# Optimization experiments

Measured on AMD Instinct MI355X. Metric: run time of the kernel, lower is better.

The kernel has to match this reference:

```python
import jax, jax.numpy as jnp
import numpy as np

TOKEN_SIZE = 4
NEIGHBOR_SIZE = 3


def setup_inputs() -> dict:
    key = jax.random.key(0)
    ks = jax.random.split(key, 8)
    B, C, H, W = 8, 256, 64, 64
    return {
        "blue_feat": jax.random.normal(ks[0], (B, C, H, W), jnp.float32),
        "white_feat": jax.random.normal(ks[1], (B, C, H, W), jnp.float32),
        "Wq": jax.random.normal(ks[2], (C, C), jnp.float32) * 0.05,
        "bq": jax.random.normal(ks[3], (C,), jnp.float32) * 0.05,
        "Wk": jax.random.normal(ks[4], (C, C), jnp.float32) * 0.05,
        "bk": jax.random.normal(ks[5], (C,), jnp.float32) * 0.05,
        "Wv": jax.random.normal(ks[6], (C, C), jnp.float32) * 0.05,
        "bv": jax.random.normal(ks[7], (C,), jnp.float32) * 0.05,
    }


def _tokens(x, nh, nw, ts):
    # [B,C,H,W] -> [B,nh,nw,C,ts*ts]
    B, C = x.shape[0], x.shape[1]
    return (x.reshape(B, C, nh, ts, nw, ts)
             .transpose(0, 2, 4, 1, 3, 5)
             .reshape(B, nh, nw, C, ts * ts))


def reference(blue_feat, white_feat, Wq, bq, Wk, bk, Wv, bv):
    ts, ns = TOKEN_SIZE, NEIGHBOR_SIZE
    pad = ns // 2
    B, C, H, W = blue_feat.shape
    scale = float((ts * ts) ** -0.5)

    # 1x1 conv projections (pointwise channel mix + bias)
    Q = jnp.einsum('bchw,oc->bohw', blue_feat, Wq) + bq[None, :, None, None]
    K = jnp.einsum('bchw,oc->bohw', white_feat, Wk) + bk[None, :, None, None]
    V = jnp.einsum('bchw,oc->bohw', white_feat, Wv) + bv[None, :, None, None]

    nh, nw = H // ts, W // ts  # H,W divisible by ts -> no padding branch
    Qt = _tokens(Q, nh, nw, ts)  # [B,nh,nw,C,D]
    Kt = _tokens(K, nh, nw, ts)
    Vt = _tokens(V, nh, nw, ts)

    # zero-padded token grid, gather 3x3 neighbor tokens (F.unfold equivalent)
    padw = ((0, 0), (pad, pad), (pad, pad), (0, 0), (0, 0))
    Kp = jnp.pad(Kt, padw)
    Vp = jnp.pad(Vt, padw)
    Knb = jnp.stack([Kp[:, di:di + nh, dj:dj + nw]
                     for di in range(ns) for dj in range(ns)], axis=3)  # [B,nh,nw,9,C,D]
    Vnb = jnp.stack([Vp[:, di:di + nh, dj:dj + nw]
                     for di in range(ns) for dj in range(ns)], axis=3)

    # per-channel attention over neighbor tokens
    attn = jax.nn.softmax(
        jnp.einsum('bhwcd,bhwncd->bhwcn', Qt, Knb) * scale, axis=-1)
    out = jnp.einsum('bhwcn,bhwncd->bhwcd', attn, Vnb)  # [B,nh,nw,C,D]

    enhanced = (out.reshape(B, nh, nw, C, ts, ts)
                   .transpose(0, 3, 1, 4, 2, 5)
                   .reshape(B, C, H, W))
    return blue_feat + enhanced  # out_proj is Identity since c1 == c2
```

## Files before the change

kernel.cpp:

```cpp
#include <hip/hip_runtime.h>
#include <hip/hip_bf16.h>
#include <stdint.h>

typedef float  f32x4  __attribute__((ext_vector_type(4)));
typedef float  f32x2  __attribute__((ext_vector_type(2)));
typedef __bf16 bf16x8 __attribute__((ext_vector_type(8)));

#define LROW 40

__global__ __launch_bounds__(256) void wprep_kernel(
    const float* __restrict__ Wq, const float* __restrict__ Wk,
    const float* __restrict__ Wv, __bf16* __restrict__ Wbf)
{
  const int wb = blockIdx.x;
  const int t  = wb >> 5;
  const float* src = (t == 0) ? Wq : (t == 1) ? Wk : Wv;
  const int off = (wb & 31) * 2048 + threadIdx.x * 8;
  f32x4 v0 = *(const f32x4*)(src + off);
  f32x4 v1 = *(const f32x4*)(src + off + 4);
  bf16x8 r;
#pragma unroll
  for (int q = 0; q < 4; ++q) { r[q] = (__bf16)v0[q]; r[q + 4] = (__bf16)v1[q]; }
  *(bf16x8*)(Wbf + t * 65536 + off) = r;
}


#define GLOAD16(GS, LD) \
  __builtin_amdgcn_global_load_lds( \
      (const __attribute__((address_space(1))) uint32_t*)(GS), \
      (__attribute__((address_space(3))) uint32_t*)(LD), 16, 0, 0)

__global__ __launch_bounds__(256) void gemm_f32lds_kernel(
    const float* __restrict__ blue, const float* __restrict__ white,
    const __bf16* __restrict__ Wbf,
    const float* __restrict__ bq, const float* __restrict__ bk,
    const float* __restrict__ bv,
    __bf16* __restrict__ Qt, __bf16* __restrict__ Kt, __bf16* __restrict__ Vt)
{
  __shared__ float  Bsf[3][32 * 128];
  __shared__ __bf16 As[3][128 * 32];

  const int bid = blockIdx.x;
  const int lid = (bid & 7) * 192 + (bid >> 3);
  const int nb  = lid / 6;
  const int bt  = lid % 6;
  const int tensor = (bt < 4) ? 1 + (bt & 1) : 0;
  const int ob     = (bt < 4) ? (bt >> 1) : (bt & 1);

  const float*  X    = (tensor == 0) ? blue : white;
  const float*  bias = (tensor == 0) ? bq : (tensor == 1) ? bk : bv;
  __bf16*       Out  = (tensor == 0) ? Qt : (tensor == 1) ? Kt : Vt;
  const __bf16* Wp   = Wbf + tensor * 65536 + ob * 32768;

  const int tid  = threadIdx.x;
  const int lane = tid & 63;
  const int w    = tid >> 6;
  const int wo   = w >> 1;
  const int wn   = w & 1;
  const int lrow = lane & 15;
  const int lks  = lane >> 4;

  const int o0    = ob * 128;
  const int n0    = nb * 128;
  const int batch = n0 >> 12;
  const int p0    = n0 & 4095;
  const int tk0   = p0 >> 4;
  const int trow  = tk0 >> 4;
  const int tcol0 = tk0 & 15;
  const float* Xb = X + (size_t)batch * (256 * 4096);

  const float* gB[4];
#pragma unroll
  for (int m = 0; m < 4; ++m) {
    const int c      = m * 4 + w;
    const int krow   = 2 * c + (lane >> 5);
    const int g      = c >> 2;
    const int px_src = ((lane & 31) * 4 + 16 * g) & 127;
    const int tl     = px_src >> 4;
    const int d      = px_src & 15;
    const int hw     = (trow * 4 + (d >> 2)) * 64 + (tcol0 + tl) * 4 + (d & 3);
    gB[m] = Xb + (size_t)krow * 4096 + hw;
  }

  const int rA    = w * 16 + (lane >> 2);
  const int gslot = (lane & 3) ^ ((lane >> 3) & 3);
  const __bf16* gA = Wp + (size_t)rA * 256 + gslot * 8;
  const int ldsOffQ0 = (w * 16) * 32;
  const int ldsOffQ1 = (64 + w * 16) * 32;

#define STAGE(BUF, KK) do {                                          \
    GLOAD16(gA + (KK) * 32,            &As[BUF][ldsOffQ0]);          \
    GLOAD16(gA + 64 * 256 + (KK) * 32, &As[BUF][ldsOffQ1]);          \
    GLOAD16(gB[0] + (size_t)(KK) * 32 * 4096, &Bsf[BUF][(0 * 4 + w) * 256]); \
    GLOAD16(gB[1] + (size_t)(KK) * 32 * 4096, &Bsf[BUF][(1 * 4 + w) * 256]); \
    GLOAD16(gB[2] + (size_t)(KK) * 32 * 4096, &Bsf[BUF][(2 * 4 + w) * 256]); \
    GLOAD16(gB[3] + (size_t)(KK) * 32 * 4096, &Bsf[BUF][(3 * 4 + w) * 256]); \
  } while (0)

  const int sxA = (lks ^ ((lrow >> 1) & 3)) * 8;
  const int pxb = wn * 64 + lrow;

  f32x4 acc[4][4];
#pragma unroll
  for (int i = 0; i < 4; ++i)
#pragma unroll
    for (int j = 0; j < 4; ++j) acc[i][j] = (f32x4)0.0f;

#define COMPUTE(BUF) do {                                                       \
    bf16x8 af[4], bfr[4];                                                       \
    _Pragma("unroll")                                                           \
    for (int i = 0; i < 4; ++i)                                                 \
      af[i] = *(const bf16x8*)&As[BUF][(wo * 64 + i * 16 + lrow) * 32 + sxA];   \
    _Pragma("unroll")                                                           \
    for (int j = 0; j < 4; ++j) {                                               \
      const int s = (pxb + j * 16 - 16 * lks + 128) & 127;                      \
      const float* bp = &Bsf[BUF][lks * 8 * 128 + s];                           \
      bf16x8 v;                                                                 \
      _Pragma("unroll")                                                         \
      for (int kk = 0; kk < 8; ++kk) v[kk] = (__bf16)bp[kk * 128];              \
      bfr[j] = v;                                                               \
    }                                                                           \
    __builtin_amdgcn_s_setprio(1);                                              \
    _Pragma("unroll")                                                           \
    for (int i = 0; i < 4; ++i)                                                 \
      _Pragma("unroll")                                                         \
      for (int j = 0; j < 4; ++j)                                               \
        acc[i][j] = __builtin_amdgcn_mfma_f32_16x16x32_bf16(af[i], bfr[j],      \
                                                            acc[i][j], 0, 0, 0);\
    __builtin_amdgcn_s_setprio(0);                                              \
  } while (0)

  STAGE(0, 0);
  STAGE(1, 1);
  STAGE(2, 2);

#define PHASE(T) do {                                                           \
    if ((T) == 7)      asm volatile("s_waitcnt vmcnt(0)"  ::: "memory");        \
    else if ((T) == 6) asm volatile("s_waitcnt vmcnt(6)"  ::: "memory");        \
    else               asm volatile("s_waitcnt vmcnt(12)" ::: "memory");        \
    __builtin_amdgcn_sched_barrier(0);                                          \
    __builtin_amdgcn_s_barrier();                                               \
    __builtin_amdgcn_sched_barrier(0);                                          \
    COMPUTE((T) % 3);                                                           \
    asm volatile("s_waitcnt lgkmcnt(0)" ::: "memory");                          \
    __builtin_amdgcn_sched_barrier(0);                                          \
    __builtin_amdgcn_s_barrier();                                               \
    __builtin_amdgcn_sched_barrier(0);                                          \
    if ((T) < 5) STAGE((T) % 3, (T) + 3);                                       \
  } while (0)

  PHASE(0); PHASE(1); PHASE(2); PHASE(3);
  PHASE(4); PHASE(5); PHASE(6); PHASE(7);
#undef PHASE
#undef STAGE
#undef COMPUTE

#pragma unroll
  for (int i = 0; i < 4; ++i) {
    const int obase = o0 + wo * 64 + i * 16 + (lane >> 4) * 4;
#pragma unroll
    for (int j = 0; j < 4; ++j) {
      const int n  = n0 + wn * 64 + j * 16 + (lane & 15);
      const int bb = n >> 12;
      const int pp = n & 4095;
      const int tt = pp >> 4;
      const int tii = tt >> 4;
      const int tjj = tt & 15;
      const int dd  = pp & 15;
      const size_t base = ((size_t)(bb * 16 + tii) * 256) * 256 + tjj * 16 + dd;
#pragma unroll
      for (int r = 0; r < 4; ++r) {
        const int o = obase + r;
        const float v = acc[i][j][r] + bias[o];
        Out[base + (size_t)o * 256] = (__bf16)v;
      }
    }
  }
}

__global__ __launch_bounds__(256) void proj_gemm_kernel(
    const float* __restrict__ blue, const float* __restrict__ white,
    const float* __restrict__ Wq, const float* __restrict__ bq,
    const float* __restrict__ Wk, const float* __restrict__ bk,
    const float* __restrict__ Wv, const float* __restrict__ bv,
    __bf16* __restrict__ Qt, __bf16* __restrict__ Kt, __bf16* __restrict__ Vt)
{
  __shared__ __bf16 As[128 * LROW];
  __shared__ __bf16 Bs[128 * LROW];

  const int bidhw = blockIdx.x;
  const int lid   = (bidhw & 7) * 192 + (bidhw >> 3);
  const int nb    = lid / 6;
  const int bt    = lid % 6;
  const int tensor = (bt < 4) ? 1 + (bt & 1) : 0;
  const int ob     = (bt < 4) ? (bt >> 1) : (bt & 1);

  const float* X    = (tensor == 0) ? blue : white;
  const float* W    = (tensor == 0) ? Wq : (tensor == 1) ? Wk : Wv;
  const float* bias = (tensor == 0) ? bq : (tensor == 1) ? bk : bv;
  __bf16*      Out  = (tensor == 0) ? Qt : (tensor == 1) ? Kt : Vt;

  const int tid  = threadIdx.x;
  const int lane = tid & 63;
  const int wave = tid >> 6;
  const int wo   = wave >> 1;
  const int wn   = wave & 1;

  const int o0 = ob * 128;
  const int n0 = nb * 128;
  const int batch = n0 >> 12;
  const int p0    = n0 & 4095;
  const int tk0   = p0 >> 4;
  const int trow  = tk0 >> 4;
  const int tcol0 = tk0 & 15;
  const float* Xb = X + (size_t)batch * (256 * 4096);

  f32x4 acc[4][4];
#pragma unroll
  for (int i = 0; i < 4; ++i)
#pragma unroll
    for (int j = 0; j < 4; ++j) acc[i][j] = (f32x4)0.0f;

  const int arow  = tid >> 1;
  const int ahalf = tid & 1;
  const int n2   = tid & 63;
  const int ko   = tid >> 6;
  const int nloc = 2 * n2;
  const int tl   = nloc >> 4;
  const int d    = nloc & 15;
  const int hw   = (trow * 4 + (d >> 2)) * 64 + (tcol0 + tl) * 4 + (d & 3);

  const int lrow = lane & 15;
  const int lk   = (lane >> 4) * 8;

  for (int kk = 0; kk < 8; ++kk) {
    const int k0 = kk * 32;
    {
      const float* src = W + (size_t)(o0 + arow) * 256 + k0 + ahalf * 16;
      f32x4 t0 = *(const f32x4*)(src + 0);
      f32x4 t1 = *(const f32x4*)(src + 4);
      f32x4 t2 = *(const f32x4*)(src + 8);
      f32x4 t3 = *(const f32x4*)(src + 12);
      bf16x8 c0, c1;
#pragma unroll
      for (int qq = 0; qq < 4; ++qq) { c0[qq] = (__bf16)t0[qq]; c0[qq + 4] = (__bf16)t1[qq]; }
#pragma unroll
      for (int qq = 0; qq < 4; ++qq) { c1[qq] = (__bf16)t2[qq]; c1[qq + 4] = (__bf16)t3[qq]; }
      __bf16* dst = As + arow * LROW + ahalf * 16;
      *(bf16x8*)(dst + 0) = c0;
      *(bf16x8*)(dst + 8) = c1;
    }
    {
      const float* src = Xb + (size_t)(k0 + ko * 8) * 4096 + hw;
      f32x2 v0 = *(const f32x2*)(src + 0 * 4096);
      f32x2 v1 = *(const f32x2*)(src + 1 * 4096);
      f32x2 v2 = *(const f32x2*)(src + 2 * 4096);
      f32x2 v3 = *(const f32x2*)(src + 3 * 4096);
      f32x2 v4 = *(const f32x2*)(src + 4 * 4096);
      f32x2 v5 = *(const f32x2*)(src + 5 * 4096);
      f32x2 v6 = *(const f32x2*)(src + 6 * 4096);
      f32x2 v7 = *(const f32x2*)(src + 7 * 4096);
      bf16x8 r0, r1;
      r0[0] = (__bf16)v0[0]; r0[1] = (__bf16)v1[0]; r0[2] = (__bf16)v2[0]; r0[3] = (__bf16)v3[0];
      r0[4] = (__bf16)v4[0]; r0[5] = (__bf16)v5[0]; r0[6] = (__bf16)v6[0]; r0[7] = (__bf16)v7[0];
      r1[0] = (__bf16)v0[1]; r1[1] = (__bf16)v1[1]; r1[2] = (__bf16)v2[1]; r1[3] = (__bf16)v3[1];
      r1[4] = (__bf16)v4[1]; r1[5] = (__bf16)v5[1]; r1[6] = (__bf16)v6[1]; r1[7] = (__bf16)v7[1];
      *(bf16x8*)(Bs + (nloc + 0) * LROW + ko * 8) = r0;
      *(bf16x8*)(Bs + (nloc + 1) * LROW + ko * 8) = r1;
    }
    __syncthreads();

    bf16x8 a[4], b[4];
#pragma unroll
    for (int i = 0; i < 4; ++i)
      a[i] = *(const bf16x8*)(As + (wo * 64 + i * 16 + lrow) * LROW + lk);
#pragma unroll
    for (int j = 0; j < 4; ++j)
      b[j] = *(const bf16x8*)(Bs + (wn * 64 + j * 16 + lrow) * LROW + lk);
#pragma unroll
    for (int i = 0; i < 4; ++i)
#pragma unroll
      for (int j = 0; j < 4; ++j)
        acc[i][j] = __builtin_amdgcn_mfma_f32_16x16x32_bf16(a[i], b[j], acc[i][j], 0, 0, 0);
    __syncthreads();
  }

#pragma unroll
  for (int i = 0; i < 4; ++i) {
    const int obase = o0 + wo * 64 + i * 16 + (lane >> 4) * 4;
#pragma unroll
    for (int j = 0; j < 4; ++j) {
      const int n  = n0 + wn * 64 + j * 16 + (lane & 15);
      const int bb = n >> 12;
      const int p  = n & 4095;
      const int tt = p >> 4;
      const int tii = tt >> 4;
      const int tjj = tt & 15;
      const int dd  = p & 15;
      const size_t base = ((size_t)(bb * 16 + tii) * 256) * 256 + tjj * 16 + dd;
#pragma unroll
      for (int r = 0; r < 4; ++r) {
        const int o = obase + r;
        const float v = acc[i][j][r] + bias[o];
        Out[base + (size_t)o * 256] = (__bf16)v;
      }
    }
  }
}

__device__ __forceinline__ void unpack8(const uint4 v, float* f) {
  const uint32_t u0 = v.x, u1 = v.y, u2 = v.z, u3 = v.w;
  f[0] = __uint_as_float(u0 << 16); f[1] = __uint_as_float(u0 & 0xffff0000u);
  f[2] = __uint_as_float(u1 << 16); f[3] = __uint_as_float(u1 & 0xffff0000u);
  f[4] = __uint_as_float(u2 << 16); f[5] = __uint_as_float(u2 & 0xffff0000u);
  f[6] = __uint_as_float(u3 << 16); f[7] = __uint_as_float(u3 & 0xffff0000u);
}

__global__ __launch_bounds__(256) void attn_kernel(
    const __bf16* __restrict__ Qt, const __bf16* __restrict__ Kt,
    const __bf16* __restrict__ Vt, const float* __restrict__ blue,
    float* __restrict__ out)
{
  const int j   = blockIdx.x;
  const int bid = (j & 7) * 256 + (j >> 3);
  const int cg  = bid & 15;
  const int ti  = (bid >> 4) & 15;
  const int b   = bid >> 8;

  const int tid = threadIdx.x;
  const int tj  = tid & 15;
  const int cl  = tid >> 4;
  const int c   = cg * 16 + cl;

  float q[16];
  {
    const __bf16* p = Qt + ((((size_t)b * 16 + ti) * 256 + c) * 16 + tj) * 16;
    unpack8(*(const uint4*)p, q);
    unpack8(*(const uint4*)(p + 8), q + 8);
  }

  float s[9];
#pragma unroll
  for (int n = 0; n < 9; ++n) {
    const int yi = ti + n / 3 - 1;
    const int yj = tj + n % 3 - 1;
    float dot = 0.0f;
    if (yi >= 0 && yi < 16 && yj >= 0 && yj < 16) {
      const __bf16* p = Kt + ((((size_t)b * 16 + yi) * 256 + c) * 16 + yj) * 16;
      float kf[16];
      unpack8(*(const uint4*)p, kf);
      unpack8(*(const uint4*)(p + 8), kf + 8);
#pragma unroll
      for (int dd = 0; dd < 16; ++dd) dot = fmaf(q[dd], kf[dd], dot);
    }
    s[n] = dot * 0.25f;
  }

  float m = s[0];
#pragma unroll
  for (int n = 1; n < 9; ++n) m = fmaxf(m, s[n]);
  float w[9], denom = 0.0f;
#pragma unroll
  for (int n = 0; n < 9; ++n) { w[n] = __expf(s[n] - m); denom += w[n]; }
  const float inv = 1.0f / denom;

  float o16[16];
#pragma unroll
  for (int dd = 0; dd < 16; ++dd) o16[dd] = 0.0f;
#pragma unroll
  for (int n = 0; n < 9; ++n) {
    const int yi = ti + n / 3 - 1;
    const int yj = tj + n % 3 - 1;
    if (yi >= 0 && yi < 16 && yj >= 0 && yj < 16) {
      const __bf16* p = Vt + ((((size_t)b * 16 + yi) * 256 + c) * 16 + yj) * 16;
      float vf[16];
      unpack8(*(const uint4*)p, vf);
      unpack8(*(const uint4*)(p + 8), vf + 8);
#pragma unroll
      for (int dd = 0; dd < 16; ++dd) o16[dd] = fmaf(w[n], vf[dd], o16[dd]);
    }
  }

  const size_t pbase = ((size_t)b * 256 + c) * 4096 + (size_t)(ti * 4) * 64 + tj * 4;
#pragma unroll
  for (int r = 0; r < 4; ++r) {
    f32x4 bl = *(const f32x4*)(blue + pbase + r * 64);
    f32x4 ov;
#pragma unroll
    for (int j2 = 0; j2 < 4; ++j2) ov[j2] = bl[j2] + o16[r * 4 + j2] * inv;
    *(f32x4*)(out + pbase + r * 64) = ov;
  }
}

extern "C" void kernel_launch(void* const* d_in, const int* in_sizes, int n_in,
                              void* d_out, int out_size, void* d_ws, size_t ws_size,
                              hipStream_t stream) {
  const float* blue  = (const float*)d_in[0];
  const float* white = (const float*)d_in[1];
  const float* Wq = (const float*)d_in[2];
  const float* bq = (const float*)d_in[3];
  const float* Wk = (const float*)d_in[4];
  const float* bk = (const float*)d_in[5];
  const float* Wv = (const float*)d_in[6];
  const float* bv = (const float*)d_in[7];
  float* out = (float*)d_out;

  const size_t tsz = (size_t)8 * 256 * 256 * 16;
  __bf16* Qt = (__bf16*)d_ws;
  __bf16* Kt = Qt + tsz;
  __bf16* Vt = Kt + tsz;

  const size_t need = (3 * tsz + 3 * 65536) * sizeof(__bf16);
  if (ws_size >= need) {
    __bf16* Wbf = Vt + tsz;
    wprep_kernel<<<96, 256, 0, stream>>>(Wq, Wk, Wv, Wbf);
    gemm_f32lds_kernel<<<1536, 256, 0, stream>>>(blue, white, Wbf, bq, bk, bv, Qt, Kt, Vt);
  } else {
    proj_gemm_kernel<<<1536, 256, 0, stream>>>(blue, white, Wq, bq, Wk, bk, Wv, bv, Qt, Kt, Vt);
  }
  attn_kernel<<<2048, 256, 0, stream>>>(Qt, Kt, Vt, blue, out);
}
```

Before: 72.69 us.

## Transpose fp32 B tile to padded bf16 LDS once per stage before MFMA

```diff
diff --git a/kernel.cpp b/kernel.cpp
--- a/kernel.cpp
+++ b/kernel.cpp
@@ -30,15 +30,16 @@
       (const __attribute__((address_space(1))) uint32_t*)(GS), \
       (__attribute__((address_space(3))) uint32_t*)(LD), 16, 0, 0)
 
-__global__ __launch_bounds__(256) void gemm_f32lds_kernel(
+__global__ __launch_bounds__(256) void gemm_fx_kernel(
     const float* __restrict__ blue, const float* __restrict__ white,
     const __bf16* __restrict__ Wbf,
     const float* __restrict__ bq, const float* __restrict__ bk,
     const float* __restrict__ bv,
     __bf16* __restrict__ Qt, __bf16* __restrict__ Kt, __bf16* __restrict__ Vt)
 {
-  __shared__ float  Bsf[3][32 * 128];
-  __shared__ __bf16 As[3][128 * 32];
+  __shared__ __bf16 As[2][128 * 32];
+  __shared__ float  Bf[3][32 * 128];
+  __shared__ __bf16 Bsb[128 * 36];
 
   const int bid = blockIdx.x;
   const int lid = (bid & 7) * 192 + (bid >> 3);
@@ -69,36 +70,54 @@
   const int tcol0 = tk0 & 15;
   const float* Xb = X + (size_t)batch * (256 * 4096);
 
-  const float* gB[4];
+  const __bf16* gA[2]; int aO[2];
+#pragma unroll
+  for (int m = 0; m < 2; ++m) {
+    const int idx  = w * 2 + m;
+    const int row  = idx * 16 + (lane >> 2);
+    const int slot = lane & 3;
+    const int ps   = slot ^ (row & 3);
+    gA[m] = Wp + (size_t)row * 256 + ps * 8;
+    aO[m] = idx * 512;
+  }
+  const float* gB[4]; int bO[4];
 #pragma unroll
   for (int m = 0; m < 4; ++m) {
-    const int c      = m * 4 + w;
-    const int krow   = 2 * c + (lane >> 5);
-    const int g      = c >> 2;
-    const int px_src = ((lane & 31) * 4 + 16 * g) & 127;
-    const int tl     = px_src >> 4;
-    const int d      = px_src & 15;
-    const int hw     = (trow * 4 + (d >> 2)) * 64 + (tcol0 + tl) * 4 + (d & 3);
+    const int c    = m * 4 + w;
+    const int krow = 2 * c + (lane >> 5);
+    const int p    = (lane & 31) * 4;
+    const int tl   = p >> 4;
+    const int d    = p & 15;
+    const int hw   = (trow * 4 + (d >> 2)) * 64 + (tcol0 + tl) * 4;
     gB[m] = Xb + (size_t)krow * 4096 + hw;
-  }
-
-  const int rA    = w * 16 + (lane >> 2);
-  const int gslot = (lane & 3) ^ ((lane >> 3) & 3);
-  const __bf16* gA = Wp + (size_t)rA * 256 + gslot * 8;
-  const int ldsOffQ0 = (w * 16) * 32;
-  const int ldsOffQ1 = (64 + w * 16) * 32;
-
-#define STAGE(BUF, KK) do {                                          \
-    GLOAD16(gA + (KK) * 32,            &As[BUF][ldsOffQ0]);          \
-    GLOAD16(gA + 64 * 256 + (KK) * 32, &As[BUF][ldsOffQ1]);          \
-    GLOAD16(gB[0] + (size_t)(KK) * 32 * 4096, &Bsf[BUF][(0 * 4 + w) * 256]); \
-    GLOAD16(gB[1] + (size_t)(KK) * 32 * 4096, &Bsf[BUF][(1 * 4 + w) * 256]); \
-    GLOAD16(gB[2] + (size_t)(KK) * 32 * 4096, &Bsf[BUF][(2 * 4 + w) * 256]); \
-    GLOAD16(gB[3] + (size_t)(KK) * 32 * 4096, &Bsf[BUF][(3 * 4 + w) * 256]); \
+    bO[m] = c * 256;
+  }
+
+#define STAGE_A(KK, BUF) do {                                  \
+    GLOAD16(gA[0] + (KK) * 32, &As[BUF][aO[0]]);               \
+    GLOAD16(gA[1] + (KK) * 32, &As[BUF][aO[1]]);               \
   } while (0)
 
-  const int sxA = (lks ^ ((lrow >> 1) & 3)) * 8;
-  const int pxb = wn * 64 + lrow;
+#define STAGE_B(KK, BUF) do {                                  \
+    GLOAD16(gB[0] + (size_t)(KK) * 32 * 4096, &Bf[BUF][bO[0]]);\
+    GLOAD16(gB[1] + (size_t)(KK) * 32 * 4096, &Bf[BUF][bO[1]]);\
+    GLOAD16(gB[2] + (size_t)(KK) * 32 * 4096, &Bf[BUF][bO[2]]);\
+    GLOAD16(gB[3] + (size_t)(KK) * 32 * 4096, &Bf[BUF][bO[3]]);\
+  } while (0)
+
+#define TRANS(BUF) do {                                                       \
+    f32x2 tv[8];                                                              \
+    _Pragma("unroll")                                                         \
+    for (int r = 0; r < 8; ++r)                                               \
+      tv[r] = *(const f32x2*)&Bf[BUF][(w * 8 + r) * 128 + 2 * lane];          \
+    bf16x8 e0, e1;                                                            \
+    _Pragma("unroll")                                                         \
+    for (int r = 0; r < 8; ++r) {                                             \
+      e0[r] = (__bf16)tv[r][0]; e1[r] = (__bf16)tv[r][1];                     \
+    }                                                                         \
+    *(bf16x8*)&Bsb[(2 * lane) * 36 + w * 8]     = e0;                         \
+    *(bf16x8*)&Bsb[(2 * lane + 1) * 36 + w * 8] = e1;                         \
+  } while (0)
 
   f32x4 acc[4][4];
 #pragma unroll
@@ -106,54 +125,55 @@
 #pragma unroll
     for (int j = 0; j < 4; ++j) acc[i][j] = (f32x4)0.0f;
 
-#define COMPUTE(BUF) do {                                                       \
-    bf16x8 af[4], bfr[4];                                                       \
-    _Pragma("unroll")                                                           \
-    for (int i = 0; i < 4; ++i)                                                 \
-      af[i] = *(const bf16x8*)&As[BUF][(wo * 64 + i * 16 + lrow) * 32 + sxA];   \
-    _Pragma("unroll")                                                           \
-    for (int j = 0; j < 4; ++j) {                                               \
-      const int s = (pxb + j * 16 - 16 * lks + 128) & 127;                      \
-      const float* bp = &Bsf[BUF][lks * 8 * 128 + s];                           \
-      bf16x8 v;                                                                 \
-      _Pragma("unroll")                                                         \
-      for (int kk = 0; kk < 8; ++kk) v[kk] = (__bf16)bp[kk * 128];              \
-      bfr[j] = v;                                                               \
-    }                                                                           \
-    __builtin_amdgcn_s_setprio(1);                                              \
-    _Pragma("unroll")                                                           \
-    for (int i = 0; i < 4; ++i)                                                 \
-      _Pragma("unroll")                                                         \
-      for (int j = 0; j < 4; ++j)                                               \
-        acc[i][j] = __builtin_amdgcn_mfma_f32_16x16x32_bf16(af[i], bfr[j],      \
-                                                            acc[i][j], 0, 0, 0);\
-    __builtin_amdgcn_s_setprio(0);                                              \
+#define COMPUTE(ABUF) do {                                                    \
+    bf16x8 af[4], bfr[4];                                                     \
+    _Pragma("unroll")                                                         \
+    for (int i = 0; i < 4; ++i) {                                             \
+      const int row = wo * 64 + i * 16 + lrow;                                \
+      af[i] = *(const bf16x8*)&As[ABUF][row * 32 + ((lks ^ (row & 3)) * 8)];  \
+    }                                                                         \
+    _Pragma("unroll")                                                         \
+    for (int j = 0; j < 4; ++j) {                                             \
+      const int px = wn * 64 + j * 16 + lrow;                                 \
+      bfr[j] = *(const bf16x8*)&Bsb[px * 36 + lks * 8];                       \
+    }                                                                         \
+    __builtin_amdgcn_s_setprio(1);                                            \
+    _Pragma("unroll")                                                         \
+    for (int i = 0; i < 4; ++i)                                               \
+      _Pragma("unroll")                                                       \
+      for (int j = 0; j < 4; ++j)                                             \
+        acc[i][j] = __builtin_amdgcn_mfma_f32_16x16x32_bf16(af[i], bfr[j],    \
+                                                            acc[i][j], 0,0,0);\
+    __builtin_amdgcn_s_setprio(0);                                            \
   } while (0)
 
-  STAGE(0, 0);
-  STAGE(1, 1);
-  STAGE(2, 2);
-
-#define PHASE(T) do {                                                           \
-    if ((T) == 7)      asm volatile("s_waitcnt vmcnt(0)"  ::: "memory");        \
-    else if ((T) == 6) asm volatile("s_waitcnt vmcnt(6)"  ::: "memory");        \
-    else               asm volatile("s_waitcnt vmcnt(12)" ::: "memory");        \
-    __builtin_amdgcn_sched_barrier(0);                                          \
-    __builtin_amdgcn_s_barrier();                                               \
-    __builtin_amdgcn_sched_barrier(0);                                          \
-    COMPUTE((T) % 3);                                                           \
-    asm volatile("s_waitcnt lgkmcnt(0)" ::: "memory");                          \
-    __builtin_amdgcn_sched_barrier(0);                                          \
-    __builtin_amdgcn_s_barrier();                                               \
-    __builtin_amdgcn_sched_barrier(0);                                          \
-    if ((T) < 5) STAGE((T) % 3, (T) + 3);                                       \
+#define PHASE(T, NW) do {                                                     \
+    asm volatile("s_waitcnt vmcnt(" #NW ")" ::: "memory");                    \
+    __builtin_amdgcn_sched_barrier(0);                                        \
+    __builtin_amdgcn_s_barrier();                                             \
+    __builtin_amdgcn_sched_barrier(0);                                        \
+    if ((T) + 1 <= 7) STAGE_A((T) + 1, ((T) + 1) & 1);                        \
+    TRANS((T) % 3);                                                           \
+    asm volatile("s_waitcnt lgkmcnt(0)" ::: "memory");                        \
+    __builtin_amdgcn_sched_barrier(0);                                        \
+    __builtin_amdgcn_s_barrier();                                             \
+    __builtin_amdgcn_sched_barrier(0);                                        \
+    COMPUTE((T) & 1);                                                         \
+    if ((T) + 3 <= 7) STAGE_B((T) + 3, ((T) + 3) % 3);                        \
   } while (0)
 
-  PHASE(0); PHASE(1); PHASE(2); PHASE(3);
-  PHASE(4); PHASE(5); PHASE(6); PHASE(7);
+  STAGE_A(0, 0);
+  STAGE_B(0, 0);
+  STAGE_B(1, 1);
+  STAGE_B(2, 2);
+
+  PHASE(0, 8); PHASE(1, 4); PHASE(2, 4); PHASE(3, 4);
+  PHASE(4, 4); PHASE(5, 4); PHASE(6, 0); PHASE(7, 0);
 #undef PHASE
-#undef STAGE
 #undef COMPUTE
+#undef TRANS
+#undef STAGE_A
+#undef STAGE_B
 
 #pragma unroll
   for (int i = 0; i < 4; ++i) {
@@ -414,7 +434,7 @@
   if (ws_size >= need) {
     __bf16* Wbf = Vt + tsz;
     wprep_kernel<<<96, 256, 0, stream>>>(Wq, Wk, Wv, Wbf);
-    gemm_f32lds_kernel<<<1536, 256, 0, stream>>>(blue, white, Wbf, bq, bk, bv, Qt, Kt, Vt);
+    gemm_fx_kernel<<<1536, 256, 0, stream>>>(blue, white, Wbf, bq, bk, bv, Qt, Kt, Vt);
   } else {
     proj_gemm_kernel<<<1536, 256, 0, stream>>>(blue, white, Wq, bq, Wk, bk, Wv, bv, Qt, Kt, Vt);
   }
```

Result: faster. 70.95 us (-2.4%).
